# Optimization experiments

Measured on AMD Instinct MI355X. Metric: run time of the kernel, lower is better.

## Reference

```python
import jax, jax.numpy as jnp
import numpy as np

N = 50000       # nodes
E = 800000      # edges
D = 128         # in_channels == hidden*heads
H = 8           # heads
C = 16          # hidden_channels (per-head dim)
L = 4           # num_layers
OUT = 128       # out_channels


def setup_inputs() -> dict:
    key = jax.random.key(0)
    ks = jax.random.split(key, 16)
    s = 1.0 / np.sqrt(D)
    inp = {
        "x": jax.random.normal(ks[0], (N, D), dtype=jnp.float32),
        "edge_index": jax.random.randint(ks[1], (2, E), 0, N, dtype=jnp.int32),
        "batch": jnp.zeros((N,), dtype=jnp.int32),
        # stacked per-layer params (all layers are D->H*C with D == H*C)
        "Wq": jax.random.normal(ks[2], (L, D, H * C), dtype=jnp.float32) * s,
        "bq": jnp.zeros((L, H * C), dtype=jnp.float32),
        "Wk": jax.random.normal(ks[3], (L, D, H * C), dtype=jnp.float32) * s,
        "bk": jnp.zeros((L, H * C), dtype=jnp.float32),
        "Wv": jax.random.normal(ks[4], (L, D, H * C), dtype=jnp.float32) * s,
        "bv": jnp.zeros((L, H * C), dtype=jnp.float32),
        "Wskip": jax.random.normal(ks[5], (L, D, H * C), dtype=jnp.float32) * s,
        "bskip": jnp.zeros((L, H * C), dtype=jnp.float32),
        "Wout": jax.random.normal(ks[6], (D, OUT), dtype=jnp.float32) * s,
        "bout": jnp.zeros((OUT,), dtype=jnp.float32),
    }
    return inp


def _transformer_conv(x, src, dst, Wq, bq, Wk, bk, Wv, bv, Wskip, bskip):
    # PyG TransformerConv (concat=True, root_weight=True, beta=False), eval mode
    q = (x @ Wq + bq).reshape(N, H, C)
    k = (x @ Wk + bk).reshape(N, H, C)
    v = (x @ Wv + bv).reshape(N, H, C)
    # edge-wise attention scores [E, H]
    score = jnp.einsum("ehc,ehc->eh", q[dst], k[src]) / jnp.sqrt(jnp.float32(C))
    # segment softmax over incoming edges of each dst node
    m = jax.ops.segment_max(score, dst, num_segments=N)          # [N, H]
    p = jnp.exp(score - m[dst])                                  # [E, H]
    z = jax.ops.segment_sum(p, dst, num_segments=N)              # [N, H]
    alpha = p / z[dst]                                           # [E, H]
    msg = alpha[:, :, None] * v[src]                             # [E, H, C]
    agg = jax.ops.segment_sum(msg, dst, num_segments=N)          # [N, H, C]
    return agg.reshape(N, H * C) + (x @ Wskip + bskip)


def reference(x, edge_index, batch, Wq, bq, Wk, bk, Wv, bv, Wskip, bskip, Wout, bout):
    src = edge_index[0]
    dst = edge_index[1]
    for l in range(L):
        x = _transformer_conv(x, src, dst, Wq[l], bq[l], Wk[l], bk[l],
                              Wv[l], bv[l], Wskip[l], bskip[l])
        x = jax.nn.relu(x)  # dropout is identity in eval mode
    return x @ Wout + bout
```

## Files before the change

kernel.cpp:

```cpp
#include <hip/hip_runtime.h>
#include <hip/hip_fp16.h>
#include <math.h>

#define NN 50000
#define EE 800000
#define DD 128

typedef __attribute__((ext_vector_type(8))) _Float16 half8;
typedef __attribute__((ext_vector_type(2))) _Float16 h2;
typedef __attribute__((ext_vector_type(4))) float f32x4;

#if __has_builtin(__builtin_amdgcn_fdot2)
#define FDOT2(a,b,c) __builtin_amdgcn_fdot2((a),(b),(c),false)
#else
static __device__ __forceinline__ float FDOT2(h2 a, h2 b, float c){
  return c + (float)a[0]*(float)b[0] + (float)a[1]*(float)b[1];
}
#endif


__global__ void zero_kernel(int* __restrict__ p, int n){
  int i = blockIdx.x*blockDim.x + threadIdx.x;
  if (i < n) p[i] = 0;
}

__global__ void hist_kernel(const int* __restrict__ edst, int* __restrict__ deg, int e){
  int i = blockIdx.x*blockDim.x + threadIdx.x;
  if (i < e) atomicAdd(&deg[edst[i]], 1);
}

__global__ void scan_partial(const int* __restrict__ deg, int* __restrict__ bsum, int n){
  __shared__ int s[256];
  int t = threadIdx.x;
  int i = blockIdx.x*256 + t;
  s[t] = (i < n) ? deg[i] : 0;
  __syncthreads();
  for (int o = 128; o > 0; o >>= 1){
    if (t < o) s[t] += s[t+o];
    __syncthreads();
  }
  if (t == 0) bsum[blockIdx.x] = s[0];
}

__global__ void scan_bsums(int* __restrict__ bsum, int nb){
  __shared__ int s[256];
  int t = threadIdx.x;
  int v = (t < nb) ? bsum[t] : 0;
  s[t] = v;
  __syncthreads();
  for (int o = 1; o < 256; o <<= 1){
    int x = (t >= o) ? s[t-o] : 0;
    __syncthreads();
    s[t] += x;
    __syncthreads();
  }
  if (t < nb) bsum[t] = s[t] - v;
}

__global__ void scan_apply(const int* __restrict__ deg, const int* __restrict__ bsum,
                           int* __restrict__ off, int* __restrict__ cursor, int n){
  __shared__ int s[256];
  int t = threadIdx.x;
  int i = blockIdx.x*256 + t;
  int v = (i < n) ? deg[i] : 0;
  s[t] = v;
  __syncthreads();
  for (int o = 1; o < 256; o <<= 1){
    int x = (t >= o) ? s[t-o] : 0;
    __syncthreads();
    s[t] += x;
    __syncthreads();
  }
  int excl = s[t] - v + bsum[blockIdx.x];
  if (i < n){
    off[i] = excl;
    if (i < n-1) cursor[i] = excl;
  }
}

__global__ void scatter_kernel(const int* __restrict__ esrc, const int* __restrict__ edst,
                               int* __restrict__ cursor, int* __restrict__ csr_src, int e){
  int i = blockIdx.x*blockDim.x + threadIdx.x;
  if (i < e){
    int d = edst[i];
    int pos = atomicAdd(&cursor[d], 1);
    csr_src[pos] = esrc[i];
  }
}

__global__ void prep_w(const float* __restrict__ Wq, const float* __restrict__ Wk,
                       const float* __restrict__ Wv, const float* __restrict__ Ws,
                       const float* __restrict__ bq, const float* __restrict__ bk,
                       const float* __restrict__ bv, const float* __restrict__ bs,
                       const float* __restrict__ Wout,
                       __half* __restrict__ wt, float* __restrict__ bcat,
                       __half* __restrict__ wtout){
  int idx = blockIdx.x*256 + threadIdx.x;
  if (idx < 4*512*128){
    int l = idx >> 16;
    int rem = idx & 65535;
    int n = rem >> 7;
    int k = rem & 127;
    int mat = n >> 7;
    int nn = n & 127;
    const float* W = (mat==0)?Wq:(mat==1)?Wk:(mat==2)?Wv:Ws;
    wt[idx] = __float2half(W[l*16384 + k*128 + nn]);
  }
  if (idx < 128*128){
    int n = idx >> 7, k = idx & 127;
    wtout[idx] = __float2half(Wout[k*128 + n]);
  }
  if (idx < 4*512){
    int l = idx >> 9, n = idx & 511;
    int mat = n >> 7, nn = n & 127;
    const float* B = (mat==0)?bq:(mat==1)?bk:(mat==2)?bv:bs;
    bcat[idx] = B[l*128 + nn];
  }
}

__global__ void convert_x(const float* __restrict__ x, __half* __restrict__ xh, int n8){
  int i = blockIdx.x*256 + threadIdx.x;
  if (i < n8){
    float4 f0 = *(const float4*)&x[(size_t)i*8];
    float4 f1 = *(const float4*)&x[(size_t)i*8+4];
    __half2 h[4] = {__floats2half2_rn(f0.x,f0.y), __floats2half2_rn(f0.z,f0.w),
                    __floats2half2_rn(f1.x,f1.y), __floats2half2_rn(f1.z,f1.w)};
    *(int4*)&xh[(size_t)i*8] = *(const int4*)h;
  }
}

template<int FMODE>
__global__ __launch_bounds__(256) void mfma_gemm(
    const __half* __restrict__ xh, const __half* __restrict__ wt,
    const float* __restrict__ bias,
    __half* __restrict__ o0, __half* __restrict__ o1,
    __half* __restrict__ o2, __half* __restrict__ o3,
    float* __restrict__ ofp, int nrows)
{
  __shared__ __half sh[32768];
  __half* a_lds = sh;
  __half* b_lds = sh + 16384;

  const int tid = threadIdx.x;
  const int m0 = blockIdx.x * 128;
  const int by = blockIdx.y;
  const int n0 = by * 128;

  #pragma unroll
  for (int p = 0; p < 8; p++){
    int chunk = tid + p*256;
    int row = chunk >> 4;
    int cs  = chunk & 15;
    int swz = cs ^ (row & 7);
    int gm = m0 + row;
    int4 va = make_int4(0,0,0,0);
    if (gm < nrows) va = *(const int4*)&xh[(size_t)gm*DD + cs*8];
    *(int4*)&a_lds[row*128 + swz*8] = va;
    int4 vb = *(const int4*)&wt[(size_t)(n0+row)*DD + cs*8];
    *(int4*)&b_lds[row*128 + swz*8] = vb;
  }
  __syncthreads();

  const int lane = tid & 63;
  const int w  = tid >> 6;
  const int wr = w >> 1, wc = w & 1;
  const int li = lane & 15, lg = lane >> 4;

  f32x4 acc[4][4];
  #pragma unroll
  for (int fn = 0; fn < 4; fn++){
    float b = bias[n0 + wc*64 + fn*16 + li];
    #pragma unroll
    for (int fm = 0; fm < 4; fm++)
      acc[fm][fn] = (f32x4){b, b, b, b};
  }

  #pragma unroll
  for (int kk = 0; kk < 4; kk++){
    half8 af[4], bf[4];
    #pragma unroll
    for (int fm = 0; fm < 4; fm++){
      int row = wr*64 + fm*16 + li;
      int chunk = kk*4 + lg;
      af[fm] = *(half8*)&a_lds[row*128 + (chunk ^ (row & 7))*8];
    }
    #pragma unroll
    for (int fn = 0; fn < 4; fn++){
      int row = wc*64 + fn*16 + li;
      int chunk = kk*4 + lg;
      bf[fn] = *(half8*)&b_lds[row*128 + (chunk ^ (row & 7))*8];
    }
    #pragma unroll
    for (int fm = 0; fm < 4; fm++)
      #pragma unroll
      for (int fn = 0; fn < 4; fn++)
        acc[fm][fn] = __builtin_amdgcn_mfma_f32_16x16x32_f16(af[fm], bf[fn], acc[fm][fn], 0, 0, 0);
  }

  if (FMODE == 0){
    __syncthreads();
    #pragma unroll
    for (int fm = 0; fm < 4; fm++)
      #pragma unroll
      for (int fn = 0; fn < 4; fn++)
        #pragma unroll
        for (int r = 0; r < 4; r++){
          int row = wr*64 + fm*16 + lg*4 + r;
          int col = wc*64 + fn*16 + li;
          int chunk = col >> 3, within = col & 7;
          a_lds[row*128 + (chunk ^ (row & 7))*8 + within] = __float2half(acc[fm][fn][r]);
        }
    __syncthreads();
    __half* dst = (by==0)?o0:(by==1)?o1:(by==2)?o2:o3;
    #pragma unroll
    for (int p = 0; p < 8; p++){
      int chunk = tid + p*256;
      int row = chunk >> 4, cs = chunk & 15;
      int gm = m0 + row;
      if (gm < nrows)
        *(int4*)&dst[(size_t)gm*DD + cs*8] = *(int4*)&a_lds[row*128 + (cs ^ (row & 7))*8];
    }
  } else {
    __syncthreads();
    float* f_lds = (float*)sh;
    #pragma unroll
    for (int fm = 0; fm < 4; fm++)
      #pragma unroll
      for (int fn = 0; fn < 4; fn++)
        #pragma unroll
        for (int r = 0; r < 4; r++){
          int row = wr*64 + fm*16 + lg*4 + r;
          int col = wc*64 + fn*16 + li;
          int chunk = col >> 2, within = col & 3;
          f_lds[row*128 + (chunk ^ (row & 7))*4 + within] = acc[fm][fn][r];
        }
    __syncthreads();
    #pragma unroll
    for (int p = 0; p < 16; p++){
      int chunk = tid + p*256;
      int row = chunk >> 5, cs = chunk & 31;
      int gm = m0 + row;
      if (gm < nrows)
        *(int4*)&ofp[(size_t)gm*DD + cs*4] = *(int4*)&f_lds[row*128 + (cs ^ (row & 7))*4];
    }
  }
}

__global__ __launch_bounds__(256) void agg_kernel(
    const __half* __restrict__ hq, const __half* __restrict__ hsk,
    const __half* __restrict__ hk, const __half* __restrict__ hv,
    const int* __restrict__ off, const int* __restrict__ csr_src,
    __half* __restrict__ xout, int n)
{
  int wid = blockIdx.x*4 + (threadIdx.x >> 6);
  if (wid >= n) return;
  int lane = threadIdx.x & 63;
  int sub  = lane >> 4;
  int c    = (lane & 15) * 8;

  h2 qv[4];
  {
    int4 qr = *(const int4*)&hq[(size_t)wid*DD + c];
    const h2* qh = (const h2*)&qr;
    qv[0]=qh[0]; qv[1]=qh[1]; qv[2]=qh[2]; qv[3]=qh[3];
  }

  float z = 0.f;
  float acc[8] = {0.f,0.f,0.f,0.f,0.f,0.f,0.f,0.f};
  const int e1 = off[wid+1];
  int e  = off[wid] + sub;
  int s2 = (e+4 < e1) ? csr_src[e+4] : -1;
  int4 kr = make_int4(0,0,0,0), vr = kr;
  if (e < e1){
    int s = csr_src[e];
    kr = *(const int4*)&hk[(size_t)s*DD + c];
    vr = *(const int4*)&hv[(size_t)s*DD + c];
  }
  while (e < e1){
    int4 kr2 = make_int4(0,0,0,0), vr2 = kr2;
    if (s2 >= 0){
      kr2 = *(const int4*)&hk[(size_t)s2*DD + c];
      vr2 = *(const int4*)&hv[(size_t)s2*DD + c];
    }
    int s3 = (e+8 < e1) ? csr_src[e+8] : -1;

    const h2* kh = (const h2*)&kr;
    float p = FDOT2(kh[0], qv[0], FDOT2(kh[1], qv[1], 0.f))
            + FDOT2(kh[2], qv[2], FDOT2(kh[3], qv[3], 0.f));
    p += __shfl_xor(p, 1);
    float wgt = __expf(p * 0.25f);
    const __half2* vh = (const __half2*)&vr;
    #pragma unroll
    for (int i = 0; i < 4; i++){
      float2 f = __half22float2(vh[i]);
      acc[2*i]   += wgt * f.x;
      acc[2*i+1] += wgt * f.y;
    }
    z += wgt;

    kr = kr2; vr = vr2; s2 = s3; e += 4;
  }

  #pragma unroll
  for (int d = 16; d <= 32; d <<= 1){
    z += __shfl_xor(z, d);
    #pragma unroll
    for (int i = 0; i < 8; i++)
      acc[i] += __shfl_xor(acc[i], d);
  }

  if (sub == 0){
    float inv = (z > 0.f) ? 1.f/z : 0.f;
    int4 sr = *(const int4*)&hsk[(size_t)wid*DD + c];
    const __half2* sh2 = (const __half2*)&sr;
    __half2 po[4];
    #pragma unroll
    for (int i = 0; i < 4; i++){
      float2 s = __half22float2(sh2[i]);
      po[i] = __floats2half2_rn(fmaxf(acc[2*i]*inv + s.x, 0.f),
                                fmaxf(acc[2*i+1]*inv + s.y, 0.f));
    }
    *(int4*)&xout[(size_t)wid*DD + c] = *(const int4*)po;
  }
}


extern "C" void kernel_launch(void* const* d_in, const int* in_sizes, int n_in,
                              void* d_out, int out_size, void* d_ws, size_t ws_size,
                              hipStream_t stream) {
  const float* x     = (const float*)d_in[0];
  const int*   edge  = (const int*)d_in[1];
  const int*   esrc  = edge;
  const int*   edst  = edge + EE;
  const float* Wq    = (const float*)d_in[3];
  const float* bq    = (const float*)d_in[4];
  const float* Wk    = (const float*)d_in[5];
  const float* bk    = (const float*)d_in[6];
  const float* Wv    = (const float*)d_in[7];
  const float* bv    = (const float*)d_in[8];
  const float* Wsk   = (const float*)d_in[9];
  const float* bsk   = (const float*)d_in[10];
  const float* Wout  = (const float*)d_in[11];
  const float* bout  = (const float*)d_in[12];
  float* out = (float*)d_out;

  uintptr_t base = (uintptr_t)d_ws;
  auto align = [](uintptr_t p){ return (p + 255) & ~(uintptr_t)255; };
  int* deg    = (int*)base;  base = align(base + (NN+1)*sizeof(int));
  int* off    = (int*)base;  base = align(base + (NN+1)*sizeof(int));
  int* cursor = (int*)base;  base = align(base + NN*sizeof(int));
  int* bsum   = (int*)base;  base = align(base + 256*sizeof(int));
  int* csr    = (int*)base;  base = align(base + (size_t)EE*sizeof(int));
  __half* xh   = (__half*)base; base = align(base + (size_t)NN*DD*sizeof(__half));
  __half* xbuf = (__half*)base; base = align(base + (size_t)NN*DD*sizeof(__half));
  __half* hq   = (__half*)base; base = align(base + (size_t)NN*DD*sizeof(__half));
  __half* hk   = (__half*)base; base = align(base + (size_t)NN*DD*sizeof(__half));
  __half* hv   = (__half*)base; base = align(base + (size_t)NN*DD*sizeof(__half));
  __half* hsk  = (__half*)base; base = align(base + (size_t)NN*DD*sizeof(__half));
  __half* wt   = (__half*)base; base = align(base + (size_t)4*512*128*sizeof(__half));
  __half* wtout= (__half*)base; base = align(base + (size_t)128*128*sizeof(__half));
  float*  bcat = (float*)base;  base = align(base + (size_t)4*512*sizeof(float));

  const int NP = NN + 1;
  const int SCAN_BLKS = (NP + 255)/256;

  zero_kernel<<<SCAN_BLKS, 256, 0, stream>>>(deg, NP);
  hist_kernel<<<(EE+255)/256, 256, 0, stream>>>(edst, deg, EE);
  scan_partial<<<SCAN_BLKS, 256, 0, stream>>>(deg, bsum, NP);
  scan_bsums<<<1, 256, 0, stream>>>(bsum, SCAN_BLKS);
  scan_apply<<<SCAN_BLKS, 256, 0, stream>>>(deg, bsum, off, cursor, NP);
  scatter_kernel<<<(EE+255)/256, 256, 0, stream>>>(esrc, edst, cursor, csr, EE);

  prep_w<<<1024, 256, 0, stream>>>(Wq, Wk, Wv, Wsk, bq, bk, bv, bsk, Wout, wt, bcat, wtout);
  convert_x<<<(NN*DD/8 + 255)/256, 256, 0, stream>>>(x, xh, NN*DD/8);

  const int MT = (NN + 127)/128;
  const __half* xin = xh;
  for (int l = 0; l < 4; l++){
    mfma_gemm<0><<<dim3(MT, 4), 256, 0, stream>>>(
        xin, wt + (size_t)l*512*128, bcat + l*512,
        hq, hk, hv, hsk, nullptr, NN);
    agg_kernel<<<(NN+3)/4, 256, 0, stream>>>(hq, hsk, hk, hv, off, csr, xbuf, NN);
    xin = xbuf;
  }
  mfma_gemm<1><<<dim3(MT, 1), 256, 0, stream>>>(
      xin, wtout, bout, nullptr, nullptr, nullptr, nullptr, out, NN);
}
```

Measured before the change: 452.0 us.

## Interleave K and V rows per node and remap aggregation lanes to one head each

The QKV GEMM now writes K and V into one interleaved buffer with a 256-half stride per node, so each gathered source node's K and V rows sit next to each other in memory. The aggregation kernel is remapped so each lane owns a whole 16-channel head and processes one of 8 edges in parallel, instead of 4 edges with half a head per lane. This removes the cross-lane shuffle for the dot product and doubles edge-level parallelism per wavefront. The cost is more registers per lane (16 accumulators, four 128-bit loads per edge) and a three-stage cross-sub reduction at the end.

```diff
diff --git a/kernel.cpp b/kernel.cpp
--- a/kernel.cpp
+++ b/kernel.cpp
@@ -133,8 +133,7 @@
 __global__ __launch_bounds__(256) void mfma_gemm(
     const __half* __restrict__ xh, const __half* __restrict__ wt,
     const float* __restrict__ bias,
-    __half* __restrict__ o0, __half* __restrict__ o1,
-    __half* __restrict__ o2, __half* __restrict__ o3,
+    __half* __restrict__ oq, __half* __restrict__ okv, __half* __restrict__ osk,
     float* __restrict__ ofp, int nrows)
 {
   __shared__ __half sh[32768];
@@ -211,14 +210,19 @@
           a_lds[row*128 + (chunk ^ (row & 7))*8 + within] = __float2half(acc[fm][fn][r]);
         }
     __syncthreads();
-    __half* dst = (by==0)?o0:(by==1)?o1:(by==2)?o2:o3;
+    __half* dst;
+    int ostride;
+    if (by == 0)      { dst = oq;        ostride = 128; }
+    else if (by == 1) { dst = okv;       ostride = 256; }
+    else if (by == 2) { dst = okv + 128; ostride = 256; }
+    else              { dst = osk;       ostride = 128; }
     #pragma unroll
     for (int p = 0; p < 8; p++){
       int chunk = tid + p*256;
       int row = chunk >> 4, cs = chunk & 15;
       int gm = m0 + row;
       if (gm < nrows)
-        *(int4*)&dst[(size_t)gm*DD + cs*8] = *(int4*)&a_lds[row*128 + (cs ^ (row & 7))*8];
+        *(int4*)&dst[(size_t)gm*ostride + cs*8] = *(int4*)&a_lds[row*128 + (cs ^ (row & 7))*8];
     }
   } else {
     __syncthreads();
@@ -248,79 +252,103 @@
 
 __global__ __launch_bounds__(256) void agg_kernel(
     const __half* __restrict__ hq, const __half* __restrict__ hsk,
-    const __half* __restrict__ hk, const __half* __restrict__ hv,
+    const __half* __restrict__ kv,
     const int* __restrict__ off, const int* __restrict__ csr_src,
     __half* __restrict__ xout, int n)
 {
   int wid = blockIdx.x*4 + (threadIdx.x >> 6);
   if (wid >= n) return;
   int lane = threadIdx.x & 63;
-  int sub  = lane >> 4;
-  int c    = (lane & 15) * 8;
-
-  h2 qv[4];
-  {
-    int4 qr = *(const int4*)&hq[(size_t)wid*DD + c];
-    const h2* qh = (const h2*)&qr;
-    qv[0]=qh[0]; qv[1]=qh[1]; qv[2]=qh[2]; qv[3]=qh[3];
-  }
+  int sub  = lane >> 3;
+  int h    = lane & 7;
+  int c    = h*16;
+
+  int4 q0 = *(const int4*)&hq[(size_t)wid*DD + c];
+  int4 q1 = *(const int4*)&hq[(size_t)wid*DD + c + 8];
 
   float z = 0.f;
-  float acc[8] = {0.f,0.f,0.f,0.f,0.f,0.f,0.f,0.f};
+  float acc[16];
+  #pragma unroll
+  for (int i = 0; i < 16; i++) acc[i] = 0.f;
+
   const int e1 = off[wid+1];
-  int e  = off[wid] + sub;
-  int s2 = (e+4 < e1) ? csr_src[e+4] : -1;
-  int4 kr = make_int4(0,0,0,0), vr = kr;
+  int e = off[wid] + sub;
+  int s2 = (e+8 < e1) ? csr_src[e+8] : -1;
+  int4 k0r, k1r, v0r, v1r;
   if (e < e1){
-    int s = csr_src[e];
-    kr = *(const int4*)&hk[(size_t)s*DD + c];
-    vr = *(const int4*)&hv[(size_t)s*DD + c];
+    const __half* r = kv + (size_t)csr_src[e]*256 + c;
+    k0r = *(const int4*)r;        k1r = *(const int4*)(r+8);
+    v0r = *(const int4*)(r+128);  v1r = *(const int4*)(r+136);
   }
   while (e < e1){
-    int4 kr2 = make_int4(0,0,0,0), vr2 = kr2;
+    int4 k0n, k1n, v0n, v1n;
     if (s2 >= 0){
-      kr2 = *(const int4*)&hk[(size_t)s2*DD + c];
-      vr2 = *(const int4*)&hv[(size_t)s2*DD + c];
-    }
-    int s3 = (e+8 < e1) ? csr_src[e+8] : -1;
-
-    const h2* kh = (const h2*)&kr;
-    float p = FDOT2(kh[0], qv[0], FDOT2(kh[1], qv[1], 0.f))
-            + FDOT2(kh[2], qv[2], FDOT2(kh[3], qv[3], 0.f));
-    p += __shfl_xor(p, 1);
+      const __half* r = kv + (size_t)s2*256 + c;
+      k0n = *(const int4*)r;        k1n = *(const int4*)(r+8);
+      v0n = *(const int4*)(r+128);  v1n = *(const int4*)(r+136);
+    }
+    int s3 = (e+16 < e1) ? csr_src[e+16] : -1;
+
+    const h2* kh0 = (const h2*)&k0r;
+    const h2* kh1 = (const h2*)&k1r;
+    const h2* qh0 = (const h2*)&q0;
+    const h2* qh1 = (const h2*)&q1;
+    float p = 0.f;
+    #pragma unroll
+    for (int i = 0; i < 4; i++) p = FDOT2(kh0[i], qh0[i], p);
+    #pragma unroll
+    for (int i = 0; i < 4; i++) p = FDOT2(kh1[i], qh1[i], p);
     float wgt = __expf(p * 0.25f);
-    const __half2* vh = (const __half2*)&vr;
+
+    const __half2* vh0 = (const __half2*)&v0r;
+    const __half2* vh1 = (const __half2*)&v1r;
     #pragma unroll
     for (int i = 0; i < 4; i++){
-      float2 f = __half22float2(vh[i]);
+      float2 f = __half22float2(vh0[i]);
       acc[2*i]   += wgt * f.x;
       acc[2*i+1] += wgt * f.y;
     }
+    #pragma unroll
+    for (int i = 0; i < 4; i++){
+      float2 f = __half22float2(vh1[i]);
+      acc[8+2*i]   += wgt * f.x;
+      acc[8+2*i+1] += wgt * f.y;
+    }
     z += wgt;
 
-    kr = kr2; vr = vr2; s2 = s3; e += 4;
+    k0r = k0n; k1r = k1n; v0r = v0n; v1r = v1n;
+    s2 = s3; e += 8;
   }
 
   #pragma unroll
-  for (int d = 16; d <= 32; d <<= 1){
+  for (int d = 8; d <= 32; d <<= 1){
     z += __shfl_xor(z, d);
     #pragma unroll
-    for (int i = 0; i < 8; i++)
+    for (int i = 0; i < 16; i++)
       acc[i] += __shfl_xor(acc[i], d);
   }
 
   if (sub == 0){
     float inv = (z > 0.f) ? 1.f/z : 0.f;
-    int4 sr = *(const int4*)&hsk[(size_t)wid*DD + c];
-    const __half2* sh2 = (const __half2*)&sr;
+    int4 s0 = *(const int4*)&hsk[(size_t)wid*DD + c];
+    int4 s1 = *(const int4*)&hsk[(size_t)wid*DD + c + 8];
+    const __half2* sh0 = (const __half2*)&s0;
+    const __half2* sh1 = (const __half2*)&s1;
     __half2 po[4];
     #pragma unroll
     for (int i = 0; i < 4; i++){
-      float2 s = __half22float2(sh2[i]);
+      float2 s = __half22float2(sh0[i]);
       po[i] = __floats2half2_rn(fmaxf(acc[2*i]*inv + s.x, 0.f),
                                 fmaxf(acc[2*i+1]*inv + s.y, 0.f));
     }
     *(int4*)&xout[(size_t)wid*DD + c] = *(const int4*)po;
+    #pragma unroll
+    for (int i = 0; i < 4; i++){
+      float2 s = __half22float2(sh1[i]);
+      po[i] = __floats2half2_rn(fmaxf(acc[8+2*i]*inv + s.x, 0.f),
+                                fmaxf(acc[8+2*i+1]*inv + s.y, 0.f));
+    }
+    *(int4*)&xout[(size_t)wid*DD + c + 8] = *(const int4*)po;
   }
 }
 
@@ -354,9 +382,8 @@
   __half* xh   = (__half*)base; base = align(base + (size_t)NN*DD*sizeof(__half));
   __half* xbuf = (__half*)base; base = align(base + (size_t)NN*DD*sizeof(__half));
   __half* hq   = (__half*)base; base = align(base + (size_t)NN*DD*sizeof(__half));
-  __half* hk   = (__half*)base; base = align(base + (size_t)NN*DD*sizeof(__half));
-  __half* hv   = (__half*)base; base = align(base + (size_t)NN*DD*sizeof(__half));
   __half* hsk  = (__half*)base; base = align(base + (size_t)NN*DD*sizeof(__half));
+  __half* kvb  = (__half*)base; base = align(base + (size_t)NN*256*sizeof(__half));
   __half* wt   = (__half*)base; base = align(base + (size_t)4*512*128*sizeof(__half));
   __half* wtout= (__half*)base; base = align(base + (size_t)128*128*sizeof(__half));
   float*  bcat = (float*)base;  base = align(base + (size_t)4*512*sizeof(float));
@@ -379,10 +406,10 @@
   for (int l = 0; l < 4; l++){
     mfma_gemm<0><<<dim3(MT, 4), 256, 0, stream>>>(
         xin, wt + (size_t)l*512*128, bcat + l*512,
-        hq, hk, hv, hsk, nullptr, NN);
-    agg_kernel<<<(NN+3)/4, 256, 0, stream>>>(hq, hsk, hk, hv, off, csr, xbuf, NN);
+        hq, kvb, hsk, nullptr, NN);
+    agg_kernel<<<(NN+3)/4, 256, 0, stream>>>(hq, hsk, kvb, off, csr, xbuf, NN);
     xin = xbuf;
   }
   mfma_gemm<1><<<dim3(MT, 1), 256, 0, stream>>>(
-      xin, wtout, bout, nullptr, nullptr, nullptr, nullptr, out, NN);
-}
+      xin, wtout, bout, nullptr, nullptr, nullptr, out, NN);
+}
```

New measurement: 455.0 us. Within noise of the previous version (+0.7%).

## Interleave K and V per node and split wave lanes between K and V

Applied to the files above, without the earlier changes.

The GEMM now writes K and V side by side into one 256-wide row per node, so each edge gather is a single contiguous 512-byte read instead of two separate 256-byte reads. The aggregation kernel is restructured so half of each 32-lane group loads K and half loads V from that row, and the attention weight is passed across with a shuffle. Each wave now handles 2 edges at a time instead of 4. The intent is better coalescing and fewer memory transactions in the gather-bound kernel, at the cost of fewer edges in flight per wave and a shallower prefetch.

```diff
diff --git a/kernel.cpp b/kernel.cpp
--- a/kernel.cpp
+++ b/kernel.cpp
@@ -133,8 +133,7 @@
 __global__ __launch_bounds__(256) void mfma_gemm(
     const __half* __restrict__ xh, const __half* __restrict__ wt,
     const float* __restrict__ bias,
-    __half* __restrict__ o0, __half* __restrict__ o1,
-    __half* __restrict__ o2, __half* __restrict__ o3,
+    __half* __restrict__ oq, __half* __restrict__ okv, __half* __restrict__ osk,
     float* __restrict__ ofp, int nrows)
 {
   __shared__ __half sh[32768];
@@ -211,14 +210,19 @@
           a_lds[row*128 + (chunk ^ (row & 7))*8 + within] = __float2half(acc[fm][fn][r]);
         }
     __syncthreads();
-    __half* dst = (by==0)?o0:(by==1)?o1:(by==2)?o2:o3;
+    __half* dst;
+    int ostride;
+    if (by == 0)      { dst = oq;        ostride = 128; }
+    else if (by == 1) { dst = okv;       ostride = 256; }
+    else if (by == 2) { dst = okv + 128; ostride = 256; }
+    else              { dst = osk;       ostride = 128; }
     #pragma unroll
     for (int p = 0; p < 8; p++){
       int chunk = tid + p*256;
       int row = chunk >> 4, cs = chunk & 15;
       int gm = m0 + row;
       if (gm < nrows)
-        *(int4*)&dst[(size_t)gm*DD + cs*8] = *(int4*)&a_lds[row*128 + (cs ^ (row & 7))*8];
+        *(int4*)&dst[(size_t)gm*ostride + cs*8] = *(int4*)&a_lds[row*128 + (cs ^ (row & 7))*8];
     }
   } else {
     __syncthreads();
@@ -248,70 +252,70 @@
 
 __global__ __launch_bounds__(256) void agg_kernel(
     const __half* __restrict__ hq, const __half* __restrict__ hsk,
-    const __half* __restrict__ hk, const __half* __restrict__ hv,
+    const __half* __restrict__ kv,
     const int* __restrict__ off, const int* __restrict__ csr_src,
     __half* __restrict__ xout, int n)
 {
   int wid = blockIdx.x*4 + (threadIdx.x >> 6);
   if (wid >= n) return;
-  int lane = threadIdx.x & 63;
-  int sub  = lane >> 4;
-  int c    = (lane & 15) * 8;
-
-  h2 qv[4];
-  {
-    int4 qr = *(const int4*)&hq[(size_t)wid*DD + c];
-    const h2* qh = (const h2*)&qr;
-    qv[0]=qh[0]; qv[1]=qh[1]; qv[2]=qh[2]; qv[3]=qh[3];
-  }
+  const int lane = threadIdx.x & 63;
+  const int half = lane >> 5;
+  const int t    = lane & 31;
+  const int isV  = t >> 4;
+  const int j    = t & 15;
+
+  int4 qr = make_int4(0,0,0,0);
+  if (!isV) qr = *(const int4*)&hq[(size_t)wid*DD + j*8];
+  const h2* qh = (const h2*)&qr;
 
   float z = 0.f;
   float acc[8] = {0.f,0.f,0.f,0.f,0.f,0.f,0.f,0.f};
+
   const int e1 = off[wid+1];
-  int e  = off[wid] + sub;
-  int s2 = (e+4 < e1) ? csr_src[e+4] : -1;
-  int4 kr = make_int4(0,0,0,0), vr = kr;
+  int e = off[wid] + half;
+  int4 cur = make_int4(0,0,0,0);
   if (e < e1){
     int s = csr_src[e];
-    kr = *(const int4*)&hk[(size_t)s*DD + c];
-    vr = *(const int4*)&hv[(size_t)s*DD + c];
+    cur = *(const int4*)&kv[(size_t)s*256 + t*8];
   }
   while (e < e1){
-    int4 kr2 = make_int4(0,0,0,0), vr2 = kr2;
-    if (s2 >= 0){
-      kr2 = *(const int4*)&hk[(size_t)s2*DD + c];
-      vr2 = *(const int4*)&hv[(size_t)s2*DD + c];
-    }
-    int s3 = (e+8 < e1) ? csr_src[e+8] : -1;
-
-    const h2* kh = (const h2*)&kr;
-    float p = FDOT2(kh[0], qv[0], FDOT2(kh[1], qv[1], 0.f))
-            + FDOT2(kh[2], qv[2], FDOT2(kh[3], qv[3], 0.f));
+    int en = e + 2;
+    int4 nxt = make_int4(0,0,0,0);
+    if (en < e1){
+      int s = csr_src[en];
+      nxt = *(const int4*)&kv[(size_t)s*256 + t*8];
+    }
+
+    const h2* kh = (const h2*)&cur;
+    float p = 0.f;
+    #pragma unroll
+    for (int i = 0; i < 4; i++) p = FDOT2(kh[i], qh[i], p);
     p += __shfl_xor(p, 1);
-    float wgt = __expf(p * 0.25f);
-    const __half2* vh = (const __half2*)&vr;
+    float w = __expf(p * 0.25f);
+    float wv = __shfl_xor(w, 16);
+
+    const __half2* vh = (const __half2*)&cur;
     #pragma unroll
     for (int i = 0; i < 4; i++){
       float2 f = __half22float2(vh[i]);
-      acc[2*i]   += wgt * f.x;
-      acc[2*i+1] += wgt * f.y;
-    }
-    z += wgt;
-
-    kr = kr2; vr = vr2; s2 = s3; e += 4;
-  }
-
+      acc[2*i]   += wv * f.x;
+      acc[2*i+1] += wv * f.y;
+    }
+    z += w;
+
+    cur = nxt;
+    e = en;
+  }
+
+  z += __shfl_xor(z, 32);
   #pragma unroll
-  for (int d = 16; d <= 32; d <<= 1){
-    z += __shfl_xor(z, d);
-    #pragma unroll
-    for (int i = 0; i < 8; i++)
-      acc[i] += __shfl_xor(acc[i], d);
-  }
-
-  if (sub == 0){
-    float inv = (z > 0.f) ? 1.f/z : 0.f;
-    int4 sr = *(const int4*)&hsk[(size_t)wid*DD + c];
+  for (int i = 0; i < 8; i++)
+    acc[i] += __shfl_xor(acc[i], 32);
+  float zb = __shfl_xor(z, 16);
+
+  if (half == 0 && isV){
+    float inv = (zb > 0.f) ? 1.f/zb : 0.f;
+    int4 sr = *(const int4*)&hsk[(size_t)wid*DD + j*8];
     const __half2* sh2 = (const __half2*)&sr;
     __half2 po[4];
     #pragma unroll
@@ -320,7 +324,7 @@
       po[i] = __floats2half2_rn(fmaxf(acc[2*i]*inv + s.x, 0.f),
                                 fmaxf(acc[2*i+1]*inv + s.y, 0.f));
     }
-    *(int4*)&xout[(size_t)wid*DD + c] = *(const int4*)po;
+    *(int4*)&xout[(size_t)wid*DD + j*8] = *(const int4*)po;
   }
 }
 
@@ -354,9 +358,8 @@
   __half* xh   = (__half*)base; base = align(base + (size_t)NN*DD*sizeof(__half));
   __half* xbuf = (__half*)base; base = align(base + (size_t)NN*DD*sizeof(__half));
   __half* hq   = (__half*)base; base = align(base + (size_t)NN*DD*sizeof(__half));
-  __half* hk   = (__half*)base; base = align(base + (size_t)NN*DD*sizeof(__half));
-  __half* hv   = (__half*)base; base = align(base + (size_t)NN*DD*sizeof(__half));
   __half* hsk  = (__half*)base; base = align(base + (size_t)NN*DD*sizeof(__half));
+  __half* kvb  = (__half*)base; base = align(base + (size_t)NN*256*sizeof(__half));
   __half* wt   = (__half*)base; base = align(base + (size_t)4*512*128*sizeof(__half));
   __half* wtout= (__half*)base; base = align(base + (size_t)128*128*sizeof(__half));
   float*  bcat = (float*)base;  base = align(base + (size_t)4*512*sizeof(float));
@@ -379,10 +382,10 @@
   for (int l = 0; l < 4; l++){
     mfma_gemm<0><<<dim3(MT, 4), 256, 0, stream>>>(
         xin, wt + (size_t)l*512*128, bcat + l*512,
-        hq, hk, hv, hsk, nullptr, NN);
-    agg_kernel<<<(NN+3)/4, 256, 0, stream>>>(hq, hsk, hk, hv, off, csr, xbuf, NN);
+        hq, kvb, hsk, nullptr, NN);
+    agg_kernel<<<(NN+3)/4, 256, 0, stream>>>(hq, hsk, kvb, off, csr, xbuf, NN);
     xin = xbuf;
   }
   mfma_gemm<1><<<dim3(MT, 1), 256, 0, stream>>>(
-      xin, wtout, bout, nullptr, nullptr, nullptr, nullptr, out, NN);
-}
+      xin, wtout, bout, nullptr, nullptr, nullptr, out, NN);
+}
```

Result: slower. 499.1 us (+10.4%).
